# Optimization experiments

Hardware: AMD Instinct MI355X
Metric: run time of the kernel (lower is better)

The kernel has to match this reference:

```python
import jax, jax.numpy as jnp
import numpy as np

N_NODES = 50000
N_EDGES = 800000
BN_EPS = 1e-5


def setup_inputs() -> dict:
    key = jax.random.key(0)
    ks = jax.random.split(key, 8)
    feat = jax.random.normal(ks[0], (N_NODES, 512), dtype=jnp.float32)
    src = jax.random.randint(ks[1], (N_EDGES,), 0, N_NODES, dtype=jnp.int32)
    dst = jax.random.randint(ks[2], (N_EDGES,), 0, N_NODES, dtype=jnp.int32)
    W0 = jax.random.normal(ks[3], (512, 128), dtype=jnp.float32) * 0.05
    W1 = jax.random.normal(ks[4], (128, 128), dtype=jnp.float32) * 0.05
    Wp1 = jax.random.normal(ks[5], (128, 256), dtype=jnp.float32) * 0.05
    bp1 = jnp.zeros((256,), dtype=jnp.float32)
    gamma = jnp.ones((256,), dtype=jnp.float32)
    beta = jnp.zeros((256,), dtype=jnp.float32)
    Wp2 = jax.random.normal(ks[6], (256, 128), dtype=jnp.float32) * 0.05
    bp2 = jnp.zeros((128,), dtype=jnp.float32)
    return {"feat": feat, "src": src, "dst": dst, "W0": W0, "W1": W1,
            "Wp1": Wp1, "bp1": bp1, "gamma": gamma, "beta": beta,
            "Wp2": Wp2, "bp2": bp2}


def reference(feat, src, dst, W0, W1, Wp1, bp1, gamma, beta, Wp2, bp2):
    N = feat.shape[0]
    # in-degrees, clamped to >=1, then D^{-1/2}
    deg = jax.ops.segment_sum(jnp.ones_like(dst, dtype=jnp.float32), dst,
                              num_segments=N)
    dinv = jnp.power(jnp.maximum(deg, 1.0), -0.5)[:, None]  # [N,1]

    def low_conv(h):
        # 2h - L_sym h = h + D^{-1/2} A D^{-1/2} h
        scaled = h * dinv
        agg = jax.ops.segment_sum(scaled[src], dst, num_segments=N)
        return h + agg * dinv

    h = low_conv(feat @ W0)      # linear0 (no bias) + conv0
    h = low_conv(h @ W1)         # linear1 (no bias) + conv1

    # MLPHead: Linear -> BatchNorm1d (training stats) -> ReLU -> Linear
    z = h @ Wp1 + bp1
    mu = jnp.mean(z, axis=0)
    var = jnp.mean((z - mu) ** 2, axis=0)  # biased var, torch training mode
    z = (z - mu) * jax.lax.rsqrt(var + BN_EPS) * gamma + beta
    z = jax.nn.relu(z)
    return z @ Wp2 + bp2
```

## Files before the change

### kernel.cpp

```cpp
#include <hip/hip_runtime.h>
#include <math.h>

constexpr int NN  = 50000;
constexpr int NE  = 800000;
constexpr int NNP = 50048;
constexpr int NB  = (NN + 255) / 256;
constexpr int GX  = NNP / 128;
constexpr int FILLB = (NE + 511) / 512;

typedef __bf16 bf16x8 __attribute__((ext_vector_type(8)));
typedef float  f32x4  __attribute__((ext_vector_type(4)));
typedef __attribute__((address_space(1))) unsigned int as1_uint;
typedef __attribute__((address_space(3))) unsigned int as3_uint;

__device__ __forceinline__ unsigned short f2bf(float x) {
    unsigned int u = __float_as_uint(x);
    return (unsigned short)((u + 0x7FFFu + ((u >> 16) & 1u)) >> 16);
}
__device__ __forceinline__ float bf2f(unsigned short h) {
    return __uint_as_float(((unsigned int)h) << 16);
}
__device__ __forceinline__ float rdlanef(float v, int j) {
    return __uint_as_float(__builtin_amdgcn_readlane(__float_as_uint(v), j));
}

__device__ __forceinline__ void gload16(const unsigned short* g, unsigned short* l) {
    __builtin_amdgcn_global_load_lds((const as1_uint*)(unsigned long long)g,
                                     (as3_uint*)(unsigned long long)l, 16, 0, 0);
}

__global__ void k_bsum(const int* __restrict__ cnt, int* __restrict__ bsum) {
    int i = blockIdx.x * 256 + threadIdx.x;
    int v = (i < NN) ? cnt[i] : 0;
#pragma unroll
    for (int off = 32; off; off >>= 1) v += __shfl_down(v, off, 64);
    __shared__ int tmp[4];
    if ((threadIdx.x & 63) == 0) tmp[threadIdx.x >> 6] = v;
    __syncthreads();
    if (threadIdx.x == 0) bsum[blockIdx.x] = tmp[0] + tmp[1] + tmp[2] + tmp[3];
}

__global__ void k_scan_bsum(const int* __restrict__ bsum, int* __restrict__ boff) {
    __shared__ int s[256];
    int t = threadIdx.x;
    int v = (t < NB) ? bsum[t] : 0;
    s[t] = v;
    __syncthreads();
    for (int off = 1; off < 256; off <<= 1) {
        int u = (t >= off) ? s[t - off] : 0;
        __syncthreads();
        s[t] += u;
        __syncthreads();
    }
    if (t < NB) boff[t] = s[t] - v;
}

__global__ void k_scan_block(const int* __restrict__ cnt, const int* __restrict__ boff,
                             int* __restrict__ rowoff, float* __restrict__ dinv) {
    __shared__ int s[256];
    int t = threadIdx.x;
    int i = blockIdx.x * 256 + t;
    int v = (i < NN) ? cnt[i] : 0;
    s[t] = v;
    __syncthreads();
    for (int off = 1; off < 256; off <<= 1) {
        int u = (t >= off) ? s[t - off] : 0;
        __syncthreads();
        s[t] += u;
        __syncthreads();
    }
    if (i < NN) {
        rowoff[i] = boff[blockIdx.x] + s[t] - v;
        dinv[i] = rsqrtf(fmaxf((float)v, 1.0f));
    }
}

__global__ __launch_bounds__(256) void k_gather_shfl(
    const unsigned short* __restrict__ HH, const float* __restrict__ dinv,
    const int* __restrict__ rowoff, const int* __restrict__ cnt,
    const int* __restrict__ eidx, unsigned short* __restrict__ OH)
{
    int node = blockIdx.x * 4 + (threadIdx.x >> 6);
    int lane = threadIdx.x & 63;
    if (node >= NNP) return;
    size_t rb = (size_t)node * 128 + lane * 2;
    if (node >= NN) {
        *reinterpret_cast<ushort2*>(&OH[rb]) = make_ushort2(0, 0);
        return;
    }
    int beg = rowoff[node], n = cnt[node];
    int c2 = lane * 2;
    float ax = 0.f, ay = 0.f;
    for (int jj = 0; jj < n; jj += 64) {
        int m = min(n - jj, 64);
        int el = (lane < m) ? eidx[beg + jj + lane] : 0;
        float dl = dinv[el];
        int j = 0;
        for (; j + 8 <= m; j += 8) {
            int s0 = __builtin_amdgcn_readlane(el, j);
            int s1 = __builtin_amdgcn_readlane(el, j + 1);
            int s2 = __builtin_amdgcn_readlane(el, j + 2);
            int s3 = __builtin_amdgcn_readlane(el, j + 3);
            int s4 = __builtin_amdgcn_readlane(el, j + 4);
            int s5 = __builtin_amdgcn_readlane(el, j + 5);
            int s6 = __builtin_amdgcn_readlane(el, j + 6);
            int s7 = __builtin_amdgcn_readlane(el, j + 7);
            ushort2 v0 = *reinterpret_cast<const ushort2*>(&HH[(size_t)s0 * 128 + c2]);
            ushort2 v1 = *reinterpret_cast<const ushort2*>(&HH[(size_t)s1 * 128 + c2]);
            ushort2 v2 = *reinterpret_cast<const ushort2*>(&HH[(size_t)s2 * 128 + c2]);
            ushort2 v3 = *reinterpret_cast<const ushort2*>(&HH[(size_t)s3 * 128 + c2]);
            ushort2 v4 = *reinterpret_cast<const ushort2*>(&HH[(size_t)s4 * 128 + c2]);
            ushort2 v5 = *reinterpret_cast<const ushort2*>(&HH[(size_t)s5 * 128 + c2]);
            ushort2 v6 = *reinterpret_cast<const ushort2*>(&HH[(size_t)s6 * 128 + c2]);
            ushort2 v7 = *reinterpret_cast<const ushort2*>(&HH[(size_t)s7 * 128 + c2]);
            float d0 = rdlanef(dl, j),     d1 = rdlanef(dl, j + 1);
            float d2 = rdlanef(dl, j + 2), d3 = rdlanef(dl, j + 3);
            float d4 = rdlanef(dl, j + 4), d5 = rdlanef(dl, j + 5);
            float d6 = rdlanef(dl, j + 6), d7 = rdlanef(dl, j + 7);
            ax = fmaf(bf2f(v0.x), d0, ax); ay = fmaf(bf2f(v0.y), d0, ay);
            ax = fmaf(bf2f(v1.x), d1, ax); ay = fmaf(bf2f(v1.y), d1, ay);
            ax = fmaf(bf2f(v2.x), d2, ax); ay = fmaf(bf2f(v2.y), d2, ay);
            ax = fmaf(bf2f(v3.x), d3, ax); ay = fmaf(bf2f(v3.y), d3, ay);
            ax = fmaf(bf2f(v4.x), d4, ax); ay = fmaf(bf2f(v4.y), d4, ay);
            ax = fmaf(bf2f(v5.x), d5, ax); ay = fmaf(bf2f(v5.y), d5, ay);
            ax = fmaf(bf2f(v6.x), d6, ax); ay = fmaf(bf2f(v6.y), d6, ay);
            ax = fmaf(bf2f(v7.x), d7, ax); ay = fmaf(bf2f(v7.y), d7, ay);
        }
        for (; j < m; ++j) {
            int s0 = __builtin_amdgcn_readlane(el, j);
            float d0 = rdlanef(dl, j);
            ushort2 v0 = *reinterpret_cast<const ushort2*>(&HH[(size_t)s0 * 128 + c2]);
            ax = fmaf(bf2f(v0.x), d0, ax); ay = fmaf(bf2f(v0.y), d0, ay);
        }
    }
    float d = dinv[node];
    ushort2 sh = *reinterpret_cast<const ushort2*>(&HH[rb]);
    float hx = fmaf(ax, d, bf2f(sh.x));
    float hy = fmaf(ay, d, bf2f(sh.y));
    *reinterpret_cast<ushort2*>(&OH[rb]) = make_ushort2(f2bf(hx), f2bf(hy));
}

__global__ void k_wprep_count(const float* __restrict__ W0, const float* __restrict__ W1,
                              const float* __restrict__ Wp1, const float* __restrict__ Wp2,
                              unsigned short* __restrict__ W0t, unsigned short* __restrict__ W1pt,
                              unsigned short* __restrict__ Wp2t, float* __restrict__ stats,
                              const int* __restrict__ dst, int* __restrict__ cnt) {
    int b = blockIdx.x, t = threadIdx.x;
    if (b >= 512) {
        int i = (b - 512) * 256 + t;
        if (i < NE) atomicAdd(&cnt[dst[i]], 1);
        return;
    }
    if (b < 128) {
        if (b < 2) stats[b * 256 + t] = 0.f;
        float s = 0.f;
        for (int k = 0; k < 128; ++k) s = fmaf(W1[b * 128 + k], Wp1[k * 256 + t], s);
        W1pt[t * 128 + b] = f2bf(s);
    } else if (b < 384) {
        int idx = (b - 128) * 256 + t;
        int k = idx >> 7, n = idx & 127;
        W0t[n * 512 + k] = f2bf(W0[idx]);
    } else {
        int idx = (b - 384) * 256 + t;
        int k = idx >> 7, n = idx & 127;
        Wp2t[n * 256 + k] = f2bf(Wp2[idx]);
    }
}

__global__ __launch_bounds__(512) void k_gemm1_fill(
    const float* __restrict__ Af, const unsigned short* __restrict__ BH,
    unsigned short* __restrict__ OHs,
    const int* __restrict__ src, const int* __restrict__ dst,
    const int* __restrict__ rowoff, int* __restrict__ cursor, int* __restrict__ eidx)
{
    if (blockIdx.x >= GX) {
        int e = (blockIdx.x - GX) * 512 + threadIdx.x;
        if (e < NE) {
            int d = dst[e];
            int p = atomicAdd(&cursor[d], 1);
            eidx[rowoff[d] + p] = src[e];
        }
        return;
    }
    constexpr int K = 512, NCOLS = 128;
    __shared__ __align__(16) unsigned short lds[2 * 4096];
    unsigned short* ldsA = lds;
    unsigned short* ldsB = lds + 4096;

    const int tid  = threadIdx.x;
    const int lane = tid & 63;
    const int wid  = tid >> 6;
    const int wm   = wid >> 1;
    const int wn   = wid & 1;
    const int row0 = blockIdx.x * 128;

    const int srow  = tid >> 2;
    const int skg   = tid & 3;
    const int skswz = skg ^ ((srow >> 1) & 3);
    const size_t aSrc = (size_t)(row0 + srow) * K + skswz * 8;
    const size_t bSrc = (size_t)srow * K + skswz * 8;

    const int frow = lane & 15;
    const int fkg  = lane >> 4;

    f32x4 acc[2][4] = {};

    for (int k0 = 0; k0 < K; k0 += 32) {
        float4 f0, f1;
        if (row0 + srow < NN) {
            const float* ap = Af + aSrc + k0;
            f0 = *reinterpret_cast<const float4*>(ap);
            f1 = *reinterpret_cast<const float4*>(ap + 4);
        } else {
            f0 = make_float4(0.f, 0.f, 0.f, 0.f);
            f1 = f0;
        }
        uint4 w;
        w.x = (unsigned)f2bf(f0.x) | ((unsigned)f2bf(f0.y) << 16);
        w.y = (unsigned)f2bf(f0.z) | ((unsigned)f2bf(f0.w) << 16);
        w.z = (unsigned)f2bf(f1.x) | ((unsigned)f2bf(f1.y) << 16);
        w.w = (unsigned)f2bf(f1.z) | ((unsigned)f2bf(f1.w) << 16);
        *reinterpret_cast<uint4*>(&ldsA[tid * 8]) = w;
        gload16(BH + bSrc + k0, ldsB + tid * 8);
        __syncthreads();

        bf16x8 a_h[2], b_h[4];
#pragma unroll
        for (int mi = 0; mi < 2; ++mi) {
            int ar  = wm * 32 + mi * 16 + frow;
            int idx = ar * 32 + ((fkg ^ ((ar >> 1) & 3)) * 8);
            a_h[mi] = *reinterpret_cast<const bf16x8*>(&ldsA[idx]);
        }
#pragma unroll
        for (int ni = 0; ni < 4; ++ni) {
            int bc  = wn * 64 + ni * 16 + frow;
            int idx = bc * 32 + ((fkg ^ ((bc >> 1) & 3)) * 8);
            b_h[ni] = *reinterpret_cast<const bf16x8*>(&ldsB[idx]);
        }
#pragma unroll
        for (int mi = 0; mi < 2; ++mi)
#pragma unroll
            for (int ni = 0; ni < 4; ++ni)
                acc[mi][ni] = __builtin_amdgcn_mfma_f32_16x16x32_bf16(a_h[mi], b_h[ni], acc[mi][ni], 0, 0, 0);
        __syncthreads();
    }

#pragma unroll
    for (int mi = 0; mi < 2; ++mi) {
        int rbase = row0 + wm * 32 + mi * 16 + (lane >> 4) * 4;
#pragma unroll
        for (int ni = 0; ni < 4; ++ni) {
            int col = wn * 64 + ni * 16 + (lane & 15);
#pragma unroll
            for (int r = 0; r < 4; ++r)
                OHs[(size_t)(rbase + r) * NCOLS + col] = f2bf(acc[mi][ni][r]);
        }
    }
}

template <int K, int NCOLS, bool BIAS, int AMODE, int OMODE, bool STATS>
__global__ __launch_bounds__(512) void k_mfma(
    const unsigned short* __restrict__ AH, const unsigned short* __restrict__ BH,
    const float* __restrict__ bias,
    const float* __restrict__ stats, const float* __restrict__ gamma,
    const float* __restrict__ beta,
    float* __restrict__ C, unsigned short* __restrict__ OHs,
    float* __restrict__ statsOut)
{
    __shared__ __align__(16) unsigned short lds[2 * 4096];
    unsigned short* ldsA = lds;
    unsigned short* ldsB = lds + 4096;

    const int tid  = threadIdx.x;
    const int lane = tid & 63;
    const int wid  = tid >> 6;
    const int wm   = wid >> 1;
    const int wn   = wid & 1;
    const int row0 = blockIdx.x * 128;
    const int col0 = blockIdx.y * 128;

    const int srow  = tid >> 2;
    const int skg   = tid & 3;
    const int skswz = skg ^ ((srow >> 1) & 3);
    const size_t aSrc = (size_t)(row0 + srow) * K + skswz * 8;
    const size_t bSrc = (size_t)(col0 + srow) * K + skswz * 8;

    const int frow = lane & 15;
    const int fkg  = lane >> 4;

    __shared__ float s_scl[256], s_shf[256];
    if constexpr (AMODE == 2) {
        if (tid < K) {
            float mu  = stats[tid] * (1.0f / NN);
            float var = stats[256 + tid] * (1.0f / NN) - mu * mu;
            float s = gamma[tid] * rsqrtf(var + 1e-5f);
            s_scl[tid] = s;
            s_shf[tid] = beta[tid] - mu * s;
        }
        __syncthreads();
    }

    f32x4 acc[2][4] = {};

    for (int k0 = 0; k0 < K; k0 += 32) {
        if constexpr (AMODE == 2) {
            uint4 raw = *reinterpret_cast<const uint4*>(&AH[aSrc + k0]);
            unsigned rw[4] = {raw.x, raw.y, raw.z, raw.w};
            int kc = k0 + skswz * 8;
            float vv[8];
#pragma unroll
            for (int q = 0; q < 8; ++q) {
                float z = bf2f((unsigned short)((q & 1) ? (rw[q >> 1] >> 16)
                                                        : (rw[q >> 1] & 0xFFFF)));
                vv[q] = fmaxf(fmaf(z, s_scl[kc + q], s_shf[kc + q]), 0.f);
            }
            uint4 w;
            w.x = (unsigned)f2bf(vv[0]) | ((unsigned)f2bf(vv[1]) << 16);
            w.y = (unsigned)f2bf(vv[2]) | ((unsigned)f2bf(vv[3]) << 16);
            w.z = (unsigned)f2bf(vv[4]) | ((unsigned)f2bf(vv[5]) << 16);
            w.w = (unsigned)f2bf(vv[6]) | ((unsigned)f2bf(vv[7]) << 16);
            *reinterpret_cast<uint4*>(&ldsA[tid * 8]) = w;
        } else {
            gload16(AH + aSrc + k0, ldsA + tid * 8);
        }
        gload16(BH + bSrc + k0, ldsB + tid * 8);
        __syncthreads();

        bf16x8 a_h[2], b_h[4];
#pragma unroll
        for (int mi = 0; mi < 2; ++mi) {
            int ar  = wm * 32 + mi * 16 + frow;
            int idx = ar * 32 + ((fkg ^ ((ar >> 1) & 3)) * 8);
            a_h[mi] = *reinterpret_cast<const bf16x8*>(&ldsA[idx]);
        }
#pragma unroll
        for (int ni = 0; ni < 4; ++ni) {
            int bc  = wn * 64 + ni * 16 + frow;
            int idx = bc * 32 + ((fkg ^ ((bc >> 1) & 3)) * 8);
            b_h[ni] = *reinterpret_cast<const bf16x8*>(&ldsB[idx]);
        }
#pragma unroll
        for (int mi = 0; mi < 2; ++mi)
#pragma unroll
            for (int ni = 0; ni < 4; ++ni)
                acc[mi][ni] = __builtin_amdgcn_mfma_f32_16x16x32_bf16(a_h[mi], b_h[ni], acc[mi][ni], 0, 0, 0);
        __syncthreads();
    }

    float psum[4] = {0.f, 0.f, 0.f, 0.f}, psq[4] = {0.f, 0.f, 0.f, 0.f};
#pragma unroll
    for (int mi = 0; mi < 2; ++mi) {
        int rbase = row0 + wm * 32 + mi * 16 + (lane >> 4) * 4;
#pragma unroll
        for (int ni = 0; ni < 4; ++ni) {
            int col = col0 + wn * 64 + ni * 16 + (lane & 15);
            float b = BIAS ? bias[col] : 0.f;
#pragma unroll
            for (int r = 0; r < 4; ++r) {
                int row = rbase + r;
                float v = acc[mi][ni][r] + b;
                if constexpr (STATS) {
                    if (row < NN) { psum[ni] += v; psq[ni] = fmaf(v, v, psq[ni]); }
                }
                if constexpr (OMODE == 1) {
                    OHs[(size_t)row * NCOLS + col] = f2bf(v);
                } else {
                    if (row < NN) C[(size_t)row * NCOLS + col] = v;
                }
            }
        }
    }

    if constexpr (STATS) {
        __shared__ float s_sum[128], s_sq[128];
        if (tid < 128) { s_sum[tid] = 0.f; s_sq[tid] = 0.f; }
        __syncthreads();
#pragma unroll
        for (int ni = 0; ni < 4; ++ni) {
            float a = psum[ni], q = psq[ni];
            a += __shfl_xor(a, 16); a += __shfl_xor(a, 32);
            q += __shfl_xor(q, 16); q += __shfl_xor(q, 32);
            if ((lane >> 4) == 0) {
                int cl = wn * 64 + ni * 16 + lane;
                atomicAdd(&s_sum[cl], a);
                atomicAdd(&s_sq[cl], q);
            }
        }
        __syncthreads();
        if (tid < 128) {
            atomicAdd(&statsOut[col0 + tid], s_sum[tid]);
            atomicAdd(&statsOut[256 + col0 + tid], s_sq[tid]);
        }
    }
}

extern "C" void kernel_launch(void* const* d_in, const int* in_sizes, int n_in,
                              void* d_out, int out_size, void* d_ws, size_t ws_size,
                              hipStream_t stream) {
    const float* feat  = (const float*)d_in[0];
    const int*   src   = (const int*)d_in[1];
    const int*   dst   = (const int*)d_in[2];
    const float* W0    = (const float*)d_in[3];
    const float* W1    = (const float*)d_in[4];
    const float* Wp1   = (const float*)d_in[5];
    const float* bp1   = (const float*)d_in[6];
    const float* gamma = (const float*)d_in[7];
    const float* beta  = (const float*)d_in[8];
    const float* Wp2   = (const float*)d_in[9];
    const float* bp2   = (const float*)d_in[10];
    float* out = (float*)d_out;

    char* wsb = (char*)d_ws;
    float* dinv   = (float*)(wsb + 4ull * 0);
    int*   cnt    = (int*)  (wsb + 4ull * 50048);
    int*   cursor = (int*)  (wsb + 4ull * 100096);
    int*   rowoff = (int*)  (wsb + 4ull * 150144);
    int*   bsum   = (int*)  (wsb + 4ull * 200192);
    int*   boff   = (int*)  (wsb + 4ull * 200448);
    int*   eidx   = (int*)  (wsb + 4ull * 200704);
    float* stats  = (float*)(wsb + 4ull * 1000704);
    unsigned short* W0t  = (unsigned short*)(wsb + 4ull * 1034496);
    unsigned short* W1pt = W0t + 65536;
    unsigned short* Wp2t = W1pt + 32768;
    unsigned short* H0 = (unsigned short*)(wsb + 4ull * 1165568);
    unsigned short* h1 = (unsigned short*)(wsb + 4ull * 4368640);
    unsigned short* h2 = H0;
    unsigned short* ZH = (unsigned short*)(wsb + 4ull * 7571712);

    hipMemsetAsync(cnt, 0, 2 * 50048 * sizeof(int), stream);
    k_wprep_count<<<512 + (NE + 255) / 256, 256, 0, stream>>>(
        W0, W1, Wp1, Wp2, W0t, W1pt, Wp2t, stats, dst, cnt);
    k_bsum<<<NB, 256, 0, stream>>>(cnt, bsum);
    k_scan_bsum<<<1, 256, 0, stream>>>(bsum, boff);
    k_scan_block<<<NB, 256, 0, stream>>>(cnt, boff, rowoff, dinv);

    k_gemm1_fill<<<GX + FILLB, 512, 0, stream>>>(
        feat, W0t, H0, src, dst, rowoff, cursor, eidx);

    k_gather_shfl<<<NNP / 4, 256, 0, stream>>>(H0, dinv, rowoff, cnt, eidx, h1);
    k_gather_shfl<<<NNP / 4, 256, 0, stream>>>(h1, dinv, rowoff, cnt, eidx, h2);

    k_mfma<128, 256, true, 0, 1, true><<<dim3(GX, 2), 512, 0, stream>>>(
        h2, W1pt, bp1, nullptr, nullptr, nullptr, nullptr, ZH, stats);

    k_mfma<256, 128, true, 2, 0, false><<<dim3(GX, 1), 512, 0, stream>>>(
        ZH, Wp2t, bp2, stats, gamma, beta, out, nullptr, nullptr);
}
```

Baseline: 215.8 us.

## Record per-edge slot during counting to drop fill atomics; pad gather loop

```diff
diff --git a/kernel.cpp b/kernel.cpp
--- a/kernel.cpp
+++ b/kernel.cpp
@@ -95,42 +95,23 @@
         int m = min(n - jj, 64);
         int el = (lane < m) ? eidx[beg + jj + lane] : 0;
         float dl = dinv[el];
-        int j = 0;
-        for (; j + 8 <= m; j += 8) {
-            int s0 = __builtin_amdgcn_readlane(el, j);
-            int s1 = __builtin_amdgcn_readlane(el, j + 1);
-            int s2 = __builtin_amdgcn_readlane(el, j + 2);
-            int s3 = __builtin_amdgcn_readlane(el, j + 3);
-            int s4 = __builtin_amdgcn_readlane(el, j + 4);
-            int s5 = __builtin_amdgcn_readlane(el, j + 5);
-            int s6 = __builtin_amdgcn_readlane(el, j + 6);
-            int s7 = __builtin_amdgcn_readlane(el, j + 7);
-            ushort2 v0 = *reinterpret_cast<const ushort2*>(&HH[(size_t)s0 * 128 + c2]);
-            ushort2 v1 = *reinterpret_cast<const ushort2*>(&HH[(size_t)s1 * 128 + c2]);
-            ushort2 v2 = *reinterpret_cast<const ushort2*>(&HH[(size_t)s2 * 128 + c2]);
-            ushort2 v3 = *reinterpret_cast<const ushort2*>(&HH[(size_t)s3 * 128 + c2]);
-            ushort2 v4 = *reinterpret_cast<const ushort2*>(&HH[(size_t)s4 * 128 + c2]);
-            ushort2 v5 = *reinterpret_cast<const ushort2*>(&HH[(size_t)s5 * 128 + c2]);
-            ushort2 v6 = *reinterpret_cast<const ushort2*>(&HH[(size_t)s6 * 128 + c2]);
-            ushort2 v7 = *reinterpret_cast<const ushort2*>(&HH[(size_t)s7 * 128 + c2]);
-            float d0 = rdlanef(dl, j),     d1 = rdlanef(dl, j + 1);
-            float d2 = rdlanef(dl, j + 2), d3 = rdlanef(dl, j + 3);
-            float d4 = rdlanef(dl, j + 4), d5 = rdlanef(dl, j + 5);
-            float d6 = rdlanef(dl, j + 6), d7 = rdlanef(dl, j + 7);
-            ax = fmaf(bf2f(v0.x), d0, ax); ay = fmaf(bf2f(v0.y), d0, ay);
-            ax = fmaf(bf2f(v1.x), d1, ax); ay = fmaf(bf2f(v1.y), d1, ay);
-            ax = fmaf(bf2f(v2.x), d2, ax); ay = fmaf(bf2f(v2.y), d2, ay);
-            ax = fmaf(bf2f(v3.x), d3, ax); ay = fmaf(bf2f(v3.y), d3, ay);
-            ax = fmaf(bf2f(v4.x), d4, ax); ay = fmaf(bf2f(v4.y), d4, ay);
-            ax = fmaf(bf2f(v5.x), d5, ax); ay = fmaf(bf2f(v5.y), d5, ay);
-            ax = fmaf(bf2f(v6.x), d6, ax); ay = fmaf(bf2f(v6.y), d6, ay);
-            ax = fmaf(bf2f(v7.x), d7, ax); ay = fmaf(bf2f(v7.y), d7, ay);
-        }
-        for (; j < m; ++j) {
-            int s0 = __builtin_amdgcn_readlane(el, j);
-            float d0 = rdlanef(dl, j);
-            ushort2 v0 = *reinterpret_cast<const ushort2*>(&HH[(size_t)s0 * 128 + c2]);
-            ax = fmaf(bf2f(v0.x), d0, ax); ay = fmaf(bf2f(v0.y), d0, ay);
+        int mp = (m + 7) & ~7;
+        for (int j = 0; j < mp; j += 8) {
+            int ss[8]; float dd[8]; ushort2 vv[8];
+#pragma unroll
+            for (int q = 0; q < 8; ++q) {
+                int jq = (j + q) & 63;
+                ss[q] = __builtin_amdgcn_readlane(el, jq);
+                dd[q] = (j + q < m) ? rdlanef(dl, jq) : 0.f;
+            }
+#pragma unroll
+            for (int q = 0; q < 8; ++q)
+                vv[q] = *reinterpret_cast<const ushort2*>(&HH[(size_t)ss[q] * 128 + c2]);
+#pragma unroll
+            for (int q = 0; q < 8; ++q) {
+                ax = fmaf(bf2f(vv[q].x), dd[q], ax);
+                ay = fmaf(bf2f(vv[q].y), dd[q], ay);
+            }
         }
     }
     float d = dinv[node];
@@ -144,11 +125,12 @@
                               const float* __restrict__ Wp1, const float* __restrict__ Wp2,
                               unsigned short* __restrict__ W0t, unsigned short* __restrict__ W1pt,
                               unsigned short* __restrict__ Wp2t, float* __restrict__ stats,
-                              const int* __restrict__ dst, int* __restrict__ cnt) {
+                              const int* __restrict__ dst, int* __restrict__ cnt,
+                              int* __restrict__ pos) {
     int b = blockIdx.x, t = threadIdx.x;
     if (b >= 512) {
         int i = (b - 512) * 256 + t;
-        if (i < NE) atomicAdd(&cnt[dst[i]], 1);
+        if (i < NE) pos[i] = atomicAdd(&cnt[dst[i]], 1);
         return;
     }
     if (b < 128) {
@@ -171,14 +153,14 @@
     const float* __restrict__ Af, const unsigned short* __restrict__ BH,
     unsigned short* __restrict__ OHs,
     const int* __restrict__ src, const int* __restrict__ dst,
-    const int* __restrict__ rowoff, int* __restrict__ cursor, int* __restrict__ eidx)
+    const int* __restrict__ rowoff, const int* __restrict__ pos,
+    int* __restrict__ eidx)
 {
     if (blockIdx.x >= GX) {
         int e = (blockIdx.x - GX) * 512 + threadIdx.x;
         if (e < NE) {
             int d = dst[e];
-            int p = atomicAdd(&cursor[d], 1);
-            eidx[rowoff[d] + p] = src[e];
+            eidx[rowoff[d] + pos[e]] = src[e];
         }
         return;
     }
@@ -413,29 +395,29 @@
     char* wsb = (char*)d_ws;
     float* dinv   = (float*)(wsb + 4ull * 0);
     int*   cnt    = (int*)  (wsb + 4ull * 50048);
-    int*   cursor = (int*)  (wsb + 4ull * 100096);
-    int*   rowoff = (int*)  (wsb + 4ull * 150144);
-    int*   bsum   = (int*)  (wsb + 4ull * 200192);
-    int*   boff   = (int*)  (wsb + 4ull * 200448);
-    int*   eidx   = (int*)  (wsb + 4ull * 200704);
-    float* stats  = (float*)(wsb + 4ull * 1000704);
-    unsigned short* W0t  = (unsigned short*)(wsb + 4ull * 1034496);
+    int*   rowoff = (int*)  (wsb + 4ull * 100096);
+    int*   bsum   = (int*)  (wsb + 4ull * 150144);
+    int*   boff   = (int*)  (wsb + 4ull * 150400);
+    int*   pos    = (int*)  (wsb + 4ull * 150656);
+    int*   eidx   = (int*)  (wsb + 4ull * 950656);
+    float* stats  = (float*)(wsb + 4ull * 1750656);
+    unsigned short* W0t  = (unsigned short*)(wsb + 4ull * 1751168);
     unsigned short* W1pt = W0t + 65536;
     unsigned short* Wp2t = W1pt + 32768;
-    unsigned short* H0 = (unsigned short*)(wsb + 4ull * 1165568);
-    unsigned short* h1 = (unsigned short*)(wsb + 4ull * 4368640);
+    unsigned short* H0 = (unsigned short*)(wsb + 4ull * 1816704);
+    unsigned short* h1 = (unsigned short*)(wsb + 4ull * 5019776);
     unsigned short* h2 = H0;
-    unsigned short* ZH = (unsigned short*)(wsb + 4ull * 7571712);
-
-    hipMemsetAsync(cnt, 0, 2 * 50048 * sizeof(int), stream);
+    unsigned short* ZH = (unsigned short*)(wsb + 4ull * 8222848);
+
+    hipMemsetAsync(cnt, 0, 50048 * sizeof(int), stream);
     k_wprep_count<<<512 + (NE + 255) / 256, 256, 0, stream>>>(
-        W0, W1, Wp1, Wp2, W0t, W1pt, Wp2t, stats, dst, cnt);
+        W0, W1, Wp1, Wp2, W0t, W1pt, Wp2t, stats, dst, cnt, pos);
     k_bsum<<<NB, 256, 0, stream>>>(cnt, bsum);
     k_scan_bsum<<<1, 256, 0, stream>>>(bsum, boff);
     k_scan_block<<<NB, 256, 0, stream>>>(cnt, boff, rowoff, dinv);
 
     k_gemm1_fill<<<GX + FILLB, 512, 0, stream>>>(
-        feat, W0t, H0, src, dst, rowoff, cursor, eidx);
+        feat, W0t, H0, src, dst, rowoff, pos, eidx);
 
     k_gather_shfl<<<NNP / 4, 256, 0, stream>>>(H0, dinv, rowoff, cnt, eidx, h1);
     k_gather_shfl<<<NNP / 4, 256, 0, stream>>>(h1, dinv, rowoff, cnt, eidx, h2);
```

New measurement: 197.1 us, median of 2. 1.09x faster.
